# Optimization experiments

Hardware: AMD Instinct MI355X
Metric: run time of the kernel (lower is better)

Reference implementation:

```python
import jax, jax.numpy as jnp
import numpy as np
from functools import partial

DOMAIN = (-1.0, 1.0)  # default domain of PiecewiseChebyshevSeries
B, X, Y, N = 16, 256, 32, 131072


def setup_inputs() -> dict:
    key = jax.random.key(0)
    k1, k2 = jax.random.split(key)
    cheb = jax.random.normal(k1, (B, X, Y), dtype=jnp.float32)
    d = DOMAIN[1] - DOMAIN[0]
    # z in [domain[0], domain[0] + X*|domain|) so z // |domain| indexes pieces in range
    z = jax.random.uniform(k2, (B, N), dtype=jnp.float32,
                           minval=DOMAIN[0], maxval=DOMAIN[0] + d * X)
    return {"z": z, "cheb": cheb}


@partial(jax.checkpoint, prevent_cse=False)
def _gather_reduce(y, cheb, x_idx):
    # y: (B, N) = arccos of disc coordinate; cheb: (B, X, Y); x_idx: (B, N) int
    Yc = cheb.shape[-1]
    basis = jnp.cos(jnp.arange(Yc, dtype=y.dtype) * y[..., None])     # (B, N, Y)
    g = jnp.take_along_axis(cheb, x_idx[..., None], axis=-2)          # (B, N, Y)
    return jnp.einsum('...m,...m->...', basis, g)                     # (B, N)


def reference(z, cheb):
    a, b = DOMAIN
    d = b - a
    # _isomorphism_to_C2: piece index and local coordinate
    x_f, y = jnp.divmod(z - a, d)
    x_idx = x_f.astype(jnp.int32)
    y = y + a
    # bijection_to_disc(y, a, b): affine map [a,b] -> [-1,1]
    y = 2.0 * (y - a) / d - 1.0
    y = jnp.arccos(y)
    return _gather_reduce(y, cheb, x_idx)
```

## Files before the change

### kernel.cpp

```cpp
#include <hip/hip_runtime.h>


constexpr int B = 16;
constexpr int X = 256;
constexpr int Y = 32;
constexpr int N = 131072;

constexpr int THREADS = 256;
constexpr int EPT = 8;
constexpr int EPB = THREADS * EPT;
constexpr int BLOCKS_PER_B = N / EPB;
constexpr int LSTR = 36;

__global__ __launch_bounds__(THREADS, 4)
void cheb_eval(const float* __restrict__ z,
               const float* __restrict__ cheb,
               float* __restrict__ out)
{
    __shared__ float lds[X * LSTR];
    const int bid   = blockIdx.x;
    const int b     = bid >> 6;
    const int chunk = bid & 63;
    const int tid   = threadIdx.x;

    const float4* src = reinterpret_cast<const float4*>(cheb + (size_t)b * (X * Y));
    #pragma unroll
    for (int k = 0; k < (X * Y / 4) / THREADS; ++k) {
        int f4  = k * THREADS + tid;
        float4 v = src[f4];
        int row = f4 >> 3;
        int q   = f4 & 7;
        *reinterpret_cast<float4*>(&lds[row * LSTR + q * 4]) = v;
    }
    __syncthreads();

    const float4* zb4 = reinterpret_cast<const float4*>(z   + (size_t)b * N + (size_t)chunk * EPB);
    float4*       ob4 = reinterpret_cast<float4*>      (out + (size_t)b * N + (size_t)chunk * EPB);

    #pragma unroll
    for (int k = 0; k < EPT / 4; ++k) {
        float4 zv = zb4[k * THREADS + tid];
        float zz[4] = {zv.x, zv.y, zv.z, zv.w};
        float r[4];
        #pragma unroll
        for (int j = 0; j < 4; ++j) {
            float u  = zz[j] + 1.0f;
            float xf = floorf(u * 0.5f);
            int   xi = (int)xf;
            float t  = fmaf(-2.0f, xf, u) - 1.0f;

            const float4* c4 = reinterpret_cast<const float4*>(&lds[xi * LSTR]);
            float t2 = t + t;

            float4 v0 = c4[0];
            float acc = fmaf(v0.y, t, v0.x);
            float Tpp = t;
            float Tp  = fmaf(t2, t, -1.0f);
            acc = fmaf(v0.z, Tp, acc);
            float Tn  = fmaf(t2, Tp, -Tpp);
            acc = fmaf(v0.w, Tn, acc);
            Tpp = Tp; Tp = Tn;

            #pragma unroll
            for (int q = 1; q < 8; ++q) {
                float4 v = c4[q];
                Tn = fmaf(t2, Tp, -Tpp); acc = fmaf(v.x, Tn, acc); Tpp = Tp; Tp = Tn;
                Tn = fmaf(t2, Tp, -Tpp); acc = fmaf(v.y, Tn, acc); Tpp = Tp; Tp = Tn;
                Tn = fmaf(t2, Tp, -Tpp); acc = fmaf(v.z, Tn, acc); Tpp = Tp; Tp = Tn;
                Tn = fmaf(t2, Tp, -Tpp); acc = fmaf(v.w, Tn, acc); Tpp = Tp; Tp = Tn;
            }
            r[j] = acc;
        }
        ob4[k * THREADS + tid] = make_float4(r[0], r[1], r[2], r[3]);
    }
}

extern "C" void kernel_launch(void* const* d_in, const int* in_sizes, int n_in,
                              void* d_out, int out_size, void* d_ws, size_t ws_size,
                              hipStream_t stream) {
    const float* z    = (const float*)d_in[0];
    const float* cheb = (const float*)d_in[1];
    float*       out  = (float*)d_out;
    dim3 grid(B * BLOCKS_PER_B);
    dim3 block(THREADS);
    hipLaunchKernelGGL(cheb_eval, grid, block, 0, stream, z, cheb, out);
}
```

Baseline: 72.78 us.

## Store Chebyshev coefficients as fp16 in LDS and halve elements per thread

Coefficients are converted to _Float16 when staged into shared memory. This halves the LDS footprint and the read bandwidth per row gather, with a row stride of 40 halves. Elements per thread drop from 8 to 4, which doubles the block count, and launch bounds rise to 8 blocks per CU for higher occupancy. The cost is fp16 rounding of the coefficients, which adds accuracy error, and each block now reloads and converts the full 32 KB coefficient table for half as many outputs.

```diff
diff --git a/kernel.cpp b/kernel.cpp
--- a/kernel.cpp
+++ b/kernel.cpp
@@ -7,20 +7,49 @@
 constexpr int N = 131072;
 
 constexpr int THREADS = 256;
-constexpr int EPT = 8;
+constexpr int EPT = 4;
 constexpr int EPB = THREADS * EPT;
 constexpr int BLOCKS_PER_B = N / EPB;
-constexpr int LSTR = 36;
+constexpr int LSTR = 40;
 
-__global__ __launch_bounds__(THREADS, 4)
+typedef _Float16 half4v __attribute__((ext_vector_type(4)));
+typedef _Float16 half8v __attribute__((ext_vector_type(8)));
+
+__device__ __forceinline__ float eval1(const _Float16* __restrict__ lds, float zj)
+{
+    float u  = zj + 1.0f;
+    float xf = floorf(u * 0.5f);
+    int   xi = (int)xf;
+    float t  = fmaf(-2.0f, xf, u) - 1.0f;
+
+    const half8v* c8 = reinterpret_cast<const half8v*>(lds + xi * LSTR);
+    half8v h[4];
+    #pragma unroll
+    for (int i = 0; i < 4; ++i) h[i] = c8[i];
+
+    float t2  = t + t;
+    float Tpp = t;
+    float acc = fmaf((float)h[0][1], t, (float)h[0][0]);
+    float Tp  = fmaf(t2, t, -1.0f);
+    acc = fmaf((float)h[0][2], Tp, acc);
+    #pragma unroll
+    for (int m = 3; m < 32; ++m) {
+        float Tn = fmaf(t2, Tp, -Tpp);
+        acc = fmaf((float)h[m >> 3][m & 7], Tn, acc);
+        Tpp = Tp; Tp = Tn;
+    }
+    return acc;
+}
+
+__global__ __launch_bounds__(THREADS, 8)
 void cheb_eval(const float* __restrict__ z,
                const float* __restrict__ cheb,
                float* __restrict__ out)
 {
-    __shared__ float lds[X * LSTR];
+    __shared__ __align__(16) _Float16 lds[X * LSTR];
     const int bid   = blockIdx.x;
-    const int b     = bid >> 6;
-    const int chunk = bid & 63;
+    const int b     = bid >> 7;
+    const int chunk = bid & 127;
     const int tid   = threadIdx.x;
 
     const float4* src = reinterpret_cast<const float4*>(cheb + (size_t)b * (X * Y));
@@ -30,49 +59,21 @@
         float4 v = src[f4];
         int row = f4 >> 3;
         int q   = f4 & 7;
-        *reinterpret_cast<float4*>(&lds[row * LSTR + q * 4]) = v;
+        half4v hv = { (_Float16)v.x, (_Float16)v.y, (_Float16)v.z, (_Float16)v.w };
+        *reinterpret_cast<half4v*>(&lds[row * LSTR + q * 4]) = hv;
     }
     __syncthreads();
 
     const float4* zb4 = reinterpret_cast<const float4*>(z   + (size_t)b * N + (size_t)chunk * EPB);
     float4*       ob4 = reinterpret_cast<float4*>      (out + (size_t)b * N + (size_t)chunk * EPB);
 
-    #pragma unroll
-    for (int k = 0; k < EPT / 4; ++k) {
-        float4 zv = zb4[k * THREADS + tid];
-        float zz[4] = {zv.x, zv.y, zv.z, zv.w};
-        float r[4];
-        #pragma unroll
-        for (int j = 0; j < 4; ++j) {
-            float u  = zz[j] + 1.0f;
-            float xf = floorf(u * 0.5f);
-            int   xi = (int)xf;
-            float t  = fmaf(-2.0f, xf, u) - 1.0f;
-
-            const float4* c4 = reinterpret_cast<const float4*>(&lds[xi * LSTR]);
-            float t2 = t + t;
-
-            float4 v0 = c4[0];
-            float acc = fmaf(v0.y, t, v0.x);
-            float Tpp = t;
-            float Tp  = fmaf(t2, t, -1.0f);
-            acc = fmaf(v0.z, Tp, acc);
-            float Tn  = fmaf(t2, Tp, -Tpp);
-            acc = fmaf(v0.w, Tn, acc);
-            Tpp = Tp; Tp = Tn;
-
-            #pragma unroll
-            for (int q = 1; q < 8; ++q) {
-                float4 v = c4[q];
-                Tn = fmaf(t2, Tp, -Tpp); acc = fmaf(v.x, Tn, acc); Tpp = Tp; Tp = Tn;
-                Tn = fmaf(t2, Tp, -Tpp); acc = fmaf(v.y, Tn, acc); Tpp = Tp; Tp = Tn;
-                Tn = fmaf(t2, Tp, -Tpp); acc = fmaf(v.z, Tn, acc); Tpp = Tp; Tp = Tn;
-                Tn = fmaf(t2, Tp, -Tpp); acc = fmaf(v.w, Tn, acc); Tpp = Tp; Tp = Tn;
-            }
-            r[j] = acc;
-        }
-        ob4[k * THREADS + tid] = make_float4(r[0], r[1], r[2], r[3]);
-    }
+    float4 zv = zb4[tid];
+    float r0, r1, r2, r3;
+    r0 = eval1(lds, zv.x);
+    r1 = eval1(lds, zv.y);
+    r2 = eval1(lds, zv.z);
+    r3 = eval1(lds, zv.w);
+    ob4[tid] = make_float4(r0, r1, r2, r3);
 }
 
 extern "C" void kernel_launch(void* const* d_in, const int* in_sizes, int n_in,
```

Measured after the change: 67.01 us. -7.9%, faster.
